# Optimization experiments

Measured on AMD Instinct MI355X. Metric: run time of the kernel, lower is better.

## Reference

```python
import jax, jax.numpy as jnp
import numpy as np

B, T, D = 2, 2048, 2048
H, KV, DH = 16, 8, 128
N, W, K = 1024, 256, 8


def rotate_half(x):
    x1, x2 = x[..., : DH // 2], x[..., DH // 2 :]
    return jnp.concatenate((-x2, x1), axis=-1)


def setup_inputs() -> dict:
    key = jax.random.key(0)
    ks = jax.random.split(key, 10)
    hidden_states = jax.random.normal(ks[0], (B, T, D), dtype=jnp.float32)
    cos = jax.random.uniform(ks[1], (B, T, DH), dtype=jnp.float32, minval=-1.0, maxval=1.0)
    sin = jax.random.uniform(ks[2], (B, T, DH), dtype=jnp.float32, minval=-1.0, maxval=1.0)
    mem = jax.random.normal(ks[3], (B, N, D), dtype=jnp.float32)
    Wq = jax.random.normal(ks[4], (D, D), dtype=jnp.float32) * 0.02
    Wk = jax.random.normal(ks[5], (KV * DH, D), dtype=jnp.float32) * 0.02
    Wv = jax.random.normal(ks[6], (KV * DH, D), dtype=jnp.float32) * 0.02
    Wo = jax.random.normal(ks[7], (D, D), dtype=jnp.float32) * 0.02
    Wg = jnp.zeros((1, D), dtype=jnp.float32)          # module inits gate weight to zeros
    bg = jnp.full((1,), 2.0, dtype=jnp.float32)        # and gate bias to 2.0
    return dict(hidden_states=hidden_states, cos=cos, sin=sin, mem=mem,
                Wq=Wq, Wk=Wk, Wv=Wv, Wo=Wo, Wg=Wg, bg=bg)


def reference(hidden_states, cos, sin, mem, Wq, Wk, Wv, Wo, Wg, bg):
    scale = DH ** -0.5
    n_rep = H // KV
    # projections -> [B, heads, T, d_h]
    q = (hidden_states @ Wq.T).reshape(B, T, H, DH).transpose(0, 2, 1, 3)
    k = (hidden_states @ Wk.T).reshape(B, T, KV, DH).transpose(0, 2, 1, 3)
    v = (hidden_states @ Wv.T).reshape(B, T, KV, DH).transpose(0, 2, 1, 3)
    # rotary (cos/sin are [B,T,d_h] -> broadcast over heads)
    c, s = cos[:, None], sin[:, None]
    q = q * c + rotate_half(q) * s
    k = k * c + rotate_half(k) * s
    # GQA repeat kv heads
    k_local = jnp.repeat(k, n_rep, axis=1)
    v_local = jnp.repeat(v, n_rep, axis=1)
    # --- local sliding-window causal attention (dense TxT mask, as in SDPA path) ---
    row = jnp.arange(T)[:, None]
    col = jnp.arange(T)[None, :]
    allowed = (col <= row) & (col >= row - W + 1)
    bias = jnp.where(allowed, 0.0, -jnp.inf).astype(q.dtype)
    scores = jnp.einsum('bhtd,bhsd->bhts', q, k_local) * scale + bias
    o_local = jnp.einsum('bhts,bhsd->bhtd', jax.nn.softmax(scores, axis=-1), v_local)
    o_local = o_local.transpose(0, 2, 1, 3).reshape(B, T, D) @ Wo.T
    # --- memory retrieval path (memory is detached in the original) ---
    mem_c = jax.lax.stop_gradient(mem)
    k_mem = (mem_c @ Wk.T).reshape(B, N, KV, DH).transpose(0, 2, 1, 3)
    v_mem = (mem_c @ Wv.T).reshape(B, N, KV, DH).transpose(0, 2, 1, 3)
    k_mem = jnp.repeat(k_mem, n_rep, axis=1)  # [B,H,N,d_h]
    v_mem = jnp.repeat(v_mem, n_rep, axis=1)
    q_chunk = q.mean(axis=2)                  # [B,H,d_h]
    sim_chunk = jnp.einsum('bhd,bhnd->bhn', q_chunk, k_mem) * scale
    _, idx = jax.lax.top_k(sim_chunk, K)      # [B,H,K]
    k_sh = jnp.take_along_axis(k_mem, idx[..., None], axis=2)  # [B,H,K,d_h]
    v_sh = jnp.take_along_axis(v_mem, idx[..., None], axis=2)
    sim_tok = jnp.einsum('bhtd,bhkd->bhtk', q, k_sh) * scale
    o_mem = jnp.einsum('bhtk,bhkd->bhtd', jax.nn.softmax(sim_tok, axis=-1), v_sh)
    o_mem = o_mem.transpose(0, 2, 1, 3).reshape(B, T, D)
    # --- learned gate fusion ---
    g = jax.nn.sigmoid(hidden_states @ Wg.T + bg)  # [B,T,1]
    return g * o_local + (1.0 - g) * o_mem
```

## Files before the change

kernel.cpp:

```cpp
#include <hip/hip_runtime.h>
#include <stdint.h>

#define B_   2
#define T_   2048
#define D_   2048
#define H_   16
#define KV_  8
#define DH_  128
#define NMEM 1024
#define WWIN 256
#define KSEL 8
#define BT   (B_*T_)
#define QKVSTR 4096

__constant__ const float kScale = 0.08838834764831845f;

typedef __attribute__((ext_vector_type(8))) short s16x8;
typedef __attribute__((ext_vector_type(4))) float f32x4;

__device__ inline unsigned short f2bf(float f) {
  union { float f; unsigned int u; } c; c.f = f;
  unsigned int u = c.u;
  unsigned int r = u + 0x7fffu + ((u >> 16) & 1u);
  return (unsigned short)(r >> 16);
}
__device__ inline float bf2f(unsigned short v) {
  union { unsigned int u; float f; } c; c.u = ((unsigned int)v) << 16;
  return c.f;
}
__device__ inline f32x4 fzero4() { f32x4 v; v[0]=0.f; v[1]=0.f; v[2]=0.f; v[3]=0.f; return v; }

__global__ __launch_bounds__(256) void conv_kernel(const float* __restrict__ src,
                                                   unsigned short* __restrict__ dst, int n) {
  int i = blockIdx.x * 256 + threadIdx.x;
  if (i * 4 >= n) return;
  float4 v = ((const float4*)src)[i];
  uint2 o;
  o.x = (unsigned)f2bf(v.x) | ((unsigned)f2bf(v.y) << 16);
  o.y = (unsigned)f2bf(v.z) | ((unsigned)f2bf(v.w) << 16);
  ((uint2*)dst)[i] = o;
}

#define AOFF(buf, half) ((buf)*32768 + (half)*16384)
#define BOFF(buf, half) (65536 + (buf)*32768 + (half)*16384)

#define PH_MFMA(P, BF) \
  { \
    _Pragma("unroll") \
    for (int mi = 0; mi < 2; ++mi) { \
      _Pragma("unroll") \
      for (int ni = 0; ni < 4; ++ni) { \
        acc[P][mi][ni] = __builtin_amdgcn_mfma_f32_16x16x32_bf16(af[mi][0], BF[ni][0], acc[P][mi][ni], 0, 0, 0); \
        acc[P][mi][ni] = __builtin_amdgcn_mfma_f32_16x16x32_bf16(af[mi][1], BF[ni][1], acc[P][mi][ni], 0, 0, 0); \
      } \
    } \
  }

template<int MODE>
__global__ __launch_bounds__(512, 2) void gemm256(const unsigned short* __restrict__ A,
                                                  const unsigned short* __restrict__ Bw,
                                                  int N, int K, int lda, int ldc,
                                                  unsigned short* __restrict__ Cb,
                                                  const float* __restrict__ g,
                                                  const unsigned short* __restrict__ omem,
                                                  float* __restrict__ dout) {
  __shared__ __align__(16) char lds[131072];
  const int tid = threadIdx.x;
  const int wv = tid >> 6, lane = tid & 63;
  const int l15 = lane & 15, lg = lane >> 4;
  const int wr = wv >> 1, wc = wv & 1;
  const int gx = gridDim.x;
  const int nwg = gx * gridDim.y;
  const int flat = blockIdx.y * gx + blockIdx.x;
  const int chunk = nwg >> 3;
  const int wg = (flat & 7) * chunk + (flat >> 3);
  const int bx = wg % gx, by = wg / gx;
  const int m0 = by * 256, n0 = bx * 256;
  const int NT = K >> 6;

  auto stage_half = [&](const unsigned short* base, int stride, int row0, int koff, int ldsoff) {
#pragma unroll
    for (int ld = 0; ld < 2; ++ld) {
      int s = ld * 512 + tid;
      int row = s >> 3, cs = s & 7;
      int cg = cs ^ (row & 7);
      const unsigned short* src = base + (size_t)(row0 + row) * stride + koff + cg * 8;
      __builtin_amdgcn_global_load_lds((const __attribute__((address_space(1))) void*)src,
          (__attribute__((address_space(3))) void*)(lds + ldsoff + ld * 8192 + wv * 1024), 16, 0, 0);
    }
  };
  auto rdA = [&](int buf, int half, int mi, int kk) -> s16x8 {
    int r = wr * 32 + mi * 16 + l15;
    int slot = (kk * 4 + lg) ^ (r & 7);
    return *(const s16x8*)(lds + AOFF(buf, half) + r * 128 + slot * 16);
  };
  auto rdB = [&](int buf, int half, int ni, int kk) -> s16x8 {
    int r = wc * 64 + ni * 16 + l15;
    int slot = (kk * 4 + lg) ^ (r & 7);
    return *(const s16x8*)(lds + BOFF(buf, half) + r * 128 + slot * 16);
  };

  f32x4 acc[4][2][4];
#pragma unroll
  for (int p = 0; p < 4; ++p)
#pragma unroll
    for (int mi = 0; mi < 2; ++mi)
#pragma unroll
      for (int ni = 0; ni < 4; ++ni) acc[p][mi][ni] = fzero4();

  stage_half(A,  lda, m0,       0,  AOFF(0, 0));
  stage_half(Bw, K,   n0,       0,  BOFF(0, 0));
  stage_half(A,  lda, m0 + 128, 0,  AOFF(0, 1));
  stage_half(Bw, K,   n0 + 128, 0,  BOFF(0, 1));
  stage_half(A,  lda, m0,       64, AOFF(1, 0));
  stage_half(Bw, K,   n0,       64, BOFF(1, 0));
  stage_half(A,  lda, m0 + 128, 64, AOFF(1, 1));
  asm volatile("s_waitcnt vmcnt(6)" ::: "memory");
  __builtin_amdgcn_s_barrier();

  int cur = 0;
  for (int t = 0; t < NT; ++t, cur ^= 1) {
    const int nxt = cur ^ 1;
    s16x8 af[2][2], b0f[4][2], b1f[4][2];
#pragma unroll
    for (int mi = 0; mi < 2; ++mi) {
      af[mi][0] = rdA(cur, 0, mi, 0);
      af[mi][1] = rdA(cur, 0, mi, 1);
    }
#pragma unroll
    for (int ni = 0; ni < 4; ++ni) {
      b0f[ni][0] = rdB(cur, 0, ni, 0);
      b0f[ni][1] = rdB(cur, 0, ni, 1);
    }
    if (t + 1 < NT) stage_half(Bw, K, n0 + 128, (t + 1) * 64, BOFF(nxt, 1));
    __builtin_amdgcn_s_barrier();
    asm volatile("s_waitcnt lgkmcnt(0)" ::: "memory");
    __builtin_amdgcn_s_setprio(1);
    PH_MFMA(0, b0f);
    __builtin_amdgcn_s_setprio(0);
    __builtin_amdgcn_s_barrier();
#pragma unroll
    for (int ni = 0; ni < 4; ++ni) {
      b1f[ni][0] = rdB(cur, 1, ni, 0);
      b1f[ni][1] = rdB(cur, 1, ni, 1);
    }
    if (t + 2 < NT) stage_half(A, lda, m0, (t + 2) * 64, AOFF(cur, 0));
    __builtin_amdgcn_s_barrier();
    asm volatile("s_waitcnt lgkmcnt(0)" ::: "memory");
    __builtin_amdgcn_s_setprio(1);
    PH_MFMA(1, b1f);
    __builtin_amdgcn_s_setprio(0);
    __builtin_amdgcn_s_barrier();
#pragma unroll
    for (int mi = 0; mi < 2; ++mi) {
      af[mi][0] = rdA(cur, 1, mi, 0);
      af[mi][1] = rdA(cur, 1, mi, 1);
    }
    if (t + 2 < NT) stage_half(Bw, K, n0, (t + 2) * 64, BOFF(cur, 0));
    __builtin_amdgcn_s_barrier();
    asm volatile("s_waitcnt lgkmcnt(0)" ::: "memory");
    __builtin_amdgcn_s_setprio(1);
    PH_MFMA(2, b0f);
    __builtin_amdgcn_s_setprio(0);
    __builtin_amdgcn_s_barrier();
    if (t + 2 < NT) stage_half(A, lda, m0 + 128, (t + 2) * 64, AOFF(cur, 1));
    __builtin_amdgcn_s_barrier();
    asm volatile("s_waitcnt lgkmcnt(0)" ::: "memory");
    __builtin_amdgcn_s_setprio(1);
    PH_MFMA(3, b1f);
    __builtin_amdgcn_s_setprio(0);
    if (t < NT - 2) asm volatile("s_waitcnt vmcnt(6)" ::: "memory");
    else            asm volatile("s_waitcnt vmcnt(0)" ::: "memory");
    __builtin_amdgcn_s_barrier();
  }

#pragma unroll
  for (int p = 0; p < 4; ++p)
#pragma unroll
    for (int mi = 0; mi < 2; ++mi)
#pragma unroll
      for (int ni = 0; ni < 4; ++ni)
#pragma unroll
        for (int j = 0; j < 4; ++j) {
          int row_g = m0 + (p >> 1) * 128 + wr * 32 + mi * 16 + lg * 4 + j;
          int col_g = n0 + (p & 1) * 128 + wc * 64 + ni * 16 + l15;
          float v = acc[p][mi][ni][j];
          size_t o = (size_t)row_g * ldc + col_g;
          if constexpr (MODE == 0) {
            Cb[o] = f2bf(v);
          } else {
            float gv = g[row_g];
            dout[o] = gv * v + (1.f - gv) * bf2f(omem[o]);
          }
        }
}

#define B2OFF(buf) (65536 + (buf)*16384)

__global__ __launch_bounds__(512, 2) void gemm256n(const unsigned short* __restrict__ A,
                                                   const unsigned short* __restrict__ Bw,
                                                   int N, int K, int lda, int ldc,
                                                   const float* __restrict__ g,
                                                   const unsigned short* __restrict__ omem,
                                                   float* __restrict__ dout) {
  __shared__ __align__(16) char lds[98304];
  const int tid = threadIdx.x;
  const int wv = tid >> 6, lane = tid & 63;
  const int l15 = lane & 15, lg = lane >> 4;
  const int wr = wv >> 1, wc = wv & 1;
  const int gx = gridDim.x;
  const int nwg = gx * gridDim.y;
  const int flat = blockIdx.y * gx + blockIdx.x;
  const int chunk = nwg >> 3;
  const int wg = (flat & 7) * chunk + (flat >> 3);
  const int bx = wg % gx, by = wg / gx;
  const int m0 = by * 256, n0 = bx * 128;
  const int NT = K >> 6;

  auto stage_half = [&](const unsigned short* base, int stride, int row0, int koff, int ldsoff) {
#pragma unroll
    for (int ld = 0; ld < 2; ++ld) {
      int s = ld * 512 + tid;
      int row = s >> 3, cs = s & 7;
      int cg = cs ^ (row & 7);
      const unsigned short* src = base + (size_t)(row0 + row) * stride + koff + cg * 8;
      __builtin_amdgcn_global_load_lds((const __attribute__((address_space(1))) void*)src,
          (__attribute__((address_space(3))) void*)(lds + ldsoff + ld * 8192 + wv * 1024), 16, 0, 0);
    }
  };
  auto rdA = [&](int buf, int half, int mi, int kk) -> s16x8 {
    int r = wr * 32 + mi * 16 + l15;
    int slot = (kk * 4 + lg) ^ (r & 7);
    return *(const s16x8*)(lds + AOFF(buf, half) + r * 128 + slot * 16);
  };
  auto rdB = [&](int buf, int ni, int kk) -> s16x8 {
    int r = wc * 64 + ni * 16 + l15;
    int slot = (kk * 4 + lg) ^ (r & 7);
    return *(const s16x8*)(lds + B2OFF(buf) + r * 128 + slot * 16);
  };

  f32x4 acc[2][2][4];
#pragma unroll
  for (int p = 0; p < 2; ++p)
#pragma unroll
    for (int mi = 0; mi < 2; ++mi)
#pragma unroll
      for (int ni = 0; ni < 4; ++ni) acc[p][mi][ni] = fzero4();

  stage_half(A,  lda, m0,       0,  AOFF(0, 0));
  stage_half(Bw, K,   n0,       0,  B2OFF(0));
  stage_half(A,  lda, m0 + 128, 0,  AOFF(0, 1));
  stage_half(A,  lda, m0,       64, AOFF(1, 0));
  stage_half(Bw, K,   n0,       64, B2OFF(1));
  asm volatile("s_waitcnt vmcnt(4)" ::: "memory");
  __builtin_amdgcn_s_barrier();

  int cur = 0;
  for (int t = 0; t < NT; ++t, cur ^= 1) {
    const int nxt = cur ^ 1;
    s16x8 af[2][2], b0f[4][2];
#pragma unroll
    for (int mi = 0; mi < 2; ++mi) {
      af[mi][0] = rdA(cur, 0, mi, 0);
      af[mi][1] = rdA(cur, 0, mi, 1);
    }
#pragma unroll
    for (int ni = 0; ni < 4; ++ni) {
      b0f[ni][0] = rdB(cur, ni, 0);
      b0f[ni][1] = rdB(cur, ni, 1);
    }
    if (t + 1 < NT) stage_half(A, lda, m0 + 128, (t + 1) * 64, AOFF(nxt, 1));
    __builtin_amdgcn_s_barrier();
    asm volatile("s_waitcnt lgkmcnt(0)" ::: "memory");
    __builtin_amdgcn_s_setprio(1);
    PH_MFMA(0, b0f);
    __builtin_amdgcn_s_setprio(0);
    __builtin_amdgcn_s_barrier();
#pragma unroll
    for (int mi = 0; mi < 2; ++mi) {
      af[mi][0] = rdA(cur, 1, mi, 0);
      af[mi][1] = rdA(cur, 1, mi, 1);
    }
    if (t + 2 < NT) {
      stage_half(A,  lda, m0, (t + 2) * 64, AOFF(cur, 0));
      stage_half(Bw, K,   n0, (t + 2) * 64, B2OFF(cur));
    }
    __builtin_amdgcn_s_barrier();
    asm volatile("s_waitcnt lgkmcnt(0)" ::: "memory");
    __builtin_amdgcn_s_setprio(1);
    PH_MFMA(1, b0f);
    __builtin_amdgcn_s_setprio(0);
    if (t < NT - 2) asm volatile("s_waitcnt vmcnt(4)" ::: "memory");
    else            asm volatile("s_waitcnt vmcnt(0)" ::: "memory");
    __builtin_amdgcn_s_barrier();
  }

#pragma unroll
  for (int p = 0; p < 2; ++p)
#pragma unroll
    for (int mi = 0; mi < 2; ++mi)
#pragma unroll
      for (int ni = 0; ni < 4; ++ni)
#pragma unroll
        for (int j = 0; j < 4; ++j) {
          int row_g = m0 + p * 128 + wr * 32 + mi * 16 + lg * 4 + j;
          int col_g = n0 + wc * 64 + ni * 16 + l15;
          float v = acc[p][mi][ni][j];
          size_t o = (size_t)row_g * ldc + col_g;
          float gv = g[row_g];
          dout[o] = gv * v + (1.f - gv) * bf2f(omem[o]);
        }
}

__global__ __launch_bounds__(256) void gsel_kernel(const unsigned short* __restrict__ mem_bf,
                                                   const unsigned short* __restrict__ wkv,
                                                   const int* __restrict__ idx,
                                                   float* __restrict__ kshp,
                                                   float* __restrict__ vshp) {
  __shared__ __align__(16) unsigned short selA[16][2056];
  __shared__ int selL[8];
  const int tid = threadIdx.x;
  const int h = blockIdx.x, b = blockIdx.y;
  const int kvh = h >> 1;
  if (tid < 8) selL[tid] = idx[(b * H_ + h) * KSEL + tid];
  __syncthreads();
#pragma unroll
  for (int it = 0; it < 8; ++it) {
    int i = it * 256 + tid;
    int r = i >> 8, c8 = i & 255;
    *(s16x8*)&selA[r][c8 * 8] =
        *(const s16x8*)(mem_bf + ((size_t)(b * NMEM + selL[r])) * D_ + c8 * 8);
  }
  {
    s16x8 z = {0, 0, 0, 0, 0, 0, 0, 0};
#pragma unroll
    for (int it = 0; it < 8; ++it) {
      int i = it * 256 + tid;
      int r = 8 + (i >> 8), c8 = i & 255;
      *(s16x8*)&selA[r][c8 * 8] = z;
    }
  }
  __syncthreads();
  const int w = tid >> 6, lane = tid & 63;
  const int l15 = lane & 15, lg = lane >> 4;
  f32x4 acc[4];
#pragma unroll
  for (int ni = 0; ni < 4; ++ni) acc[ni] = fzero4();
  const unsigned short* brow[4];
#pragma unroll
  for (int ni = 0; ni < 4; ++ni) {
    int col = w * 64 + ni * 16 + l15;
    brow[ni] = (col < 128)
        ? (wkv + (size_t)(kvh * DH_ + col) * D_)
        : (wkv + (size_t)(KV_ * DH_ + kvh * DH_ + (col - 128)) * D_);
  }
  for (int kt = 0; kt < D_ / 32; ++kt) {
    s16x8 af = *(const s16x8*)&selA[l15][kt * 32 + lg * 8];
#pragma unroll
    for (int ni = 0; ni < 4; ++ni) {
      s16x8 bf_ = *(const s16x8*)(brow[ni] + kt * 32 + lg * 8);
      acc[ni] = __builtin_amdgcn_mfma_f32_16x16x32_bf16(af, bf_, acc[ni], 0, 0, 0);
    }
  }
#pragma unroll
  for (int ni = 0; ni < 4; ++ni)
#pragma unroll
    for (int j = 0; j < 4; ++j) {
      int row = lg * 4 + j;
      int col = w * 64 + ni * 16 + l15;
      if (row < 8) {
        float* outp = (col < 128 ? kshp : vshp) +
                      ((size_t)(b * H_ + h) * KSEL + row) * DH_ + (col & 127);
        *outp = acc[ni][j];
      }
    }
}

__global__ __launch_bounds__(256) void rope_ip_kernel(unsigned short* __restrict__ buf,
                                                      const float* __restrict__ cosp,
                                                      const float* __restrict__ sinp,
                                                      int logp, int stride, int nthreads) {
  int i = blockIdx.x * 256 + threadIdx.x;
  if (i >= nthreads) return;
  int pp = i * 8;
  int row = pp >> logp;
  int p0 = pp & ((1 << logp) - 1);
  int blk = p0 >> 6, dd0 = p0 & 63;
  int b = row >> 11, t = row & 2047;
  const float* cb = cosp + ((size_t)b * T_ + t) * DH_;
  const float* sb = sinp + ((size_t)b * T_ + t) * DH_;
  unsigned short* p1 = buf + (size_t)row * stride + blk * 128 + dd0;
  s16x8 a = *(s16x8*)p1;
  s16x8 b8 = *(s16x8*)(p1 + 64);
  s16x8 o1, o2;
#pragma unroll
  for (int e = 0; e < 8; ++e) {
    float c1 = cb[dd0 + e], s1 = sb[dd0 + e];
    float c2 = cb[dd0 + 64 + e], s2 = sb[dd0 + 64 + e];
    float x1 = bf2f((unsigned short)a[e]), x2 = bf2f((unsigned short)b8[e]);
    o1[e] = (short)f2bf(x1 * c1 - x2 * s1);
    o2[e] = (short)f2bf(x2 * c2 + x1 * s2);
  }
  *(s16x8*)p1 = o1;
  *(s16x8*)(p1 + 64) = o2;
}

__global__ __launch_bounds__(256) void cs_kernel(const float* __restrict__ hs,
                                                 const float* __restrict__ cosp,
                                                 const float* __restrict__ sinp,
                                                 float* __restrict__ Cp, float* __restrict__ Sp) {
  __shared__ __align__(16) float hsL[32][128];
  __shared__ __align__(16) float csL[32][32];
  __shared__ __align__(16) float snL[32][32];
  const int tid = threadIdx.x;
  const int j0 = blockIdx.x * 128, d0 = blockIdx.y * 32;
  const int b = blockIdx.z >> 3, sp = blockIdx.z & 7;
  const int dq = (tid & 7) * 4;
  const int jq = (tid >> 3) * 4;
  float4 aC[4], aS[4];
#pragma unroll
  for (int a = 0; a < 4; ++a) {
    aC[a] = make_float4(0.f, 0.f, 0.f, 0.f);
    aS[a] = make_float4(0.f, 0.f, 0.f, 0.f);
  }
  const int csrow = tid >> 3, csc4 = tid & 7;
  for (int tile = 0; tile < 8; ++tile) {
    int t0 = sp * 256 + tile * 32;
    const float4* hs4 = (const float4*)(hs + ((size_t)b * T_ + t0) * D_ + j0);
#pragma unroll
    for (int r = 0; r < 4; ++r) {
      int i = tid + r * 256;
      int row = i >> 5, c4 = i & 31;
      *(float4*)&hsL[row][c4 * 4] = hs4[(size_t)row * (D_ / 4) + c4];
    }
    const float4* cp4 = (const float4*)(cosp + ((size_t)b * T_ + t0) * DH_ + d0);
    const float4* sp4 = (const float4*)(sinp + ((size_t)b * T_ + t0) * DH_ + d0);
    *(float4*)&csL[csrow][csc4 * 4] = cp4[(size_t)csrow * (DH_ / 4) + csc4];
    *(float4*)&snL[csrow][csc4 * 4] = sp4[(size_t)csrow * (DH_ / 4) + csc4];
    __syncthreads();
#pragma unroll 8
    for (int tt = 0; tt < 32; ++tt) {
      float4 cv = *(const float4*)&csL[tt][dq];
      float4 sv = *(const float4*)&snL[tt][dq];
      float4 hv = *(const float4*)&hsL[tt][jq];
      float ca[4] = {cv.x, cv.y, cv.z, cv.w};
      float sa[4] = {sv.x, sv.y, sv.z, sv.w};
#pragma unroll
      for (int a = 0; a < 4; ++a) {
        aC[a].x += ca[a] * hv.x; aC[a].y += ca[a] * hv.y;
        aC[a].z += ca[a] * hv.z; aC[a].w += ca[a] * hv.w;
        aS[a].x += sa[a] * hv.x; aS[a].y += sa[a] * hv.y;
        aS[a].z += sa[a] * hv.z; aS[a].w += sa[a] * hv.w;
      }
    }
    __syncthreads();
  }
#pragma unroll
  for (int a = 0; a < 4; ++a) {
    size_t o = ((size_t)(sp * B_ + b) * DH_ + d0 + dq + a) * D_ + j0 + jq;
    *(float4*)&Cp[o] = aC[a];
    *(float4*)&Sp[o] = aS[a];
  }
}

__global__ __launch_bounds__(256) void reduce_cs_kernel(const float4* __restrict__ Cp,
                                                        const float4* __restrict__ Sp,
                                                        float4* __restrict__ Cr,
                                                        float4* __restrict__ Sr) {
  int i = blockIdx.x * 256 + threadIdx.x;
  const int str = (B_ * DH_ * D_) / 4;
  float4 c = Cp[i], s = Sp[i];
#pragma unroll
  for (int p = 1; p < 8; ++p) {
    float4 cp = Cp[i + (size_t)p * str], sq = Sp[i + (size_t)p * str];
    c.x += cp.x; c.y += cp.y; c.z += cp.z; c.w += cp.w;
    s.x += sq.x; s.y += sq.y; s.z += sq.z; s.w += sq.w;
  }
  Cr[i] = c; Sr[i] = s;
}

__global__ __launch_bounds__(256) void qchunk_kernel(const float* __restrict__ Wq,
                                                     const float* __restrict__ Cr,
                                                     const float* __restrict__ Sr,
                                                     float* __restrict__ qc) {
  int gid = blockIdx.x * 256 + threadIdx.x;
  int wid = gid >> 6, lane = gid & 63;
  int b = wid >> 11, rem = wid & 2047;
  int h = rem >> 7, d = rem & 127;
  const float* w1 = Wq + (size_t)(h * DH_ + d) * D_;
  int dp = (d < 64) ? d + 64 : d - 64;
  float sgn = (d < 64) ? -1.f : 1.f;
  const float* w2 = Wq + (size_t)(h * DH_ + dp) * D_;
  const float* crow = Cr + ((size_t)b * DH_ + d) * D_;
  const float* srow = Sr + ((size_t)b * DH_ + d) * D_;
  float a1 = 0.f, a2 = 0.f;
  for (int j = lane; j < D_; j += 64) { a1 += w1[j] * crow[j]; a2 += w2[j] * srow[j]; }
#pragma unroll
  for (int off = 1; off < 64; off <<= 1) { a1 += __shfl_xor(a1, off); a2 += __shfl_xor(a2, off); }
  if (lane == 0) qc[wid] = (a1 + sgn * a2) * (1.f / (float)T_);
}

__global__ __launch_bounds__(256) void zk_kernel(const float* __restrict__ qc,
                                                 const float* __restrict__ Wk,
                                                 float* __restrict__ z) {
  int j = blockIdx.x * 256 + threadIdx.x;
  int h = blockIdx.y, b = blockIdx.z;
  int kvh = h >> 1;
  const float* qcl = qc + ((size_t)b * H_ + h) * DH_;
  const float* wb = Wk + (size_t)kvh * DH_ * D_ + j;
  float acc = 0.f;
#pragma unroll 8
  for (int d = 0; d < 128; ++d) acc += qcl[d] * wb[(size_t)d * D_];
  z[((size_t)b * H_ + h) * D_ + j] = acc;
}

__global__ __launch_bounds__(256) void sim_kernel(const float* __restrict__ z,
                                                  const float* __restrict__ mem,
                                                  float* __restrict__ sim) {
  __shared__ float4 mL[16 * 512];
  int tid = threadIdx.x;
  int n0 = blockIdx.x * 16, b = blockIdx.y;
  const float4* mem4 = (const float4*)(mem + (size_t)b * NMEM * D_);
#pragma unroll
  for (int c = 0; c < 32; ++c) {
    int i = tid + c * 256;
    int r = i >> 9, j4 = i & 511;
    mL[r * 512 + (j4 ^ (r & 7))] = mem4[(size_t)(n0 + r) * 512 + j4];
  }
  __syncthreads();
  int h = tid >> 4, n = tid & 15;
  const float4* zr = (const float4*)(z + ((size_t)b * H_ + h) * D_);
  float acc = 0.f;
  for (int j4 = 0; j4 < 512; ++j4) {
    float4 zz = zr[j4];
    float4 mm = mL[n * 512 + (j4 ^ (n & 7))];
    acc += zz.x * mm.x + zz.y * mm.y + zz.z * mm.z + zz.w * mm.w;
  }
  sim[((size_t)b * H_ + h) * NMEM + n0 + n] = acc * kScale;
}

__global__ __launch_bounds__(256) void topk_kernel(const float* __restrict__ sim,
                                                   int* __restrict__ idx) {
  __shared__ float sL[1024];
  __shared__ float rv[256];
  __shared__ int ri[256];
  int tid = threadIdx.x;
  int h = blockIdx.x, b = blockIdx.y;
  const float* sp = sim + ((size_t)b * H_ + h) * NMEM;
#pragma unroll
  for (int r = 0; r < 4; ++r) sL[tid + r * 256] = sp[tid + r * 256];
  __syncthreads();
  for (int kk = 0; kk < 8; ++kk) {
    float bv = -INFINITY; int bi = 0x7fffffff;
#pragma unroll
    for (int r = 0; r < 4; ++r) {
      int i = tid + r * 256;
      float v = sL[i];
      if (v > bv || (v == bv && i < bi)) { bv = v; bi = i; }
    }
    rv[tid] = bv; ri[tid] = bi;
    __syncthreads();
    for (int s = 128; s > 0; s >>= 1) {
      if (tid < s) {
        float v2 = rv[tid + s]; int i2 = ri[tid + s];
        if (v2 > rv[tid] || (v2 == rv[tid] && i2 < ri[tid])) { rv[tid] = v2; ri[tid] = i2; }
      }
      __syncthreads();
    }
    if (tid == 0) { idx[((size_t)b * H_ + h) * KSEL + kk] = ri[0]; sL[ri[0]] = -INFINITY; }
    __syncthreads();
  }
}

__global__ __launch_bounds__(256) void memattn_kernel(const unsigned short* __restrict__ qbf,
                                                      const float* __restrict__ ksh,
                                                      const float* __restrict__ vsh,
                                                      unsigned short* __restrict__ omem) {
  __shared__ float kl[8][128];
  __shared__ float vl[8][128];
  int tid = threadIdx.x;
  int b = blockIdx.z, h = blockIdx.y, t = blockIdx.x * 256 + tid;
  const float* ks = ksh + ((size_t)b * H_ + h) * KSEL * DH_;
  const float* vs = vsh + ((size_t)b * H_ + h) * KSEL * DH_;
#pragma unroll
  for (int r = 0; r < 4; ++r) {
    int i = tid + r * 256;
    ((float*)kl)[i] = ks[i];
    ((float*)vl)[i] = vs[i];
  }
  __syncthreads();
  float sc[8] = {0.f,0.f,0.f,0.f,0.f,0.f,0.f,0.f};
  const unsigned short* qr = qbf + (size_t)(b * T_ + t) * QKVSTR + h * DH_;
  for (int c = 0; c < 4; ++c) {
    const s16x8* qp = (const s16x8*)(qr + c * 32);
#pragma unroll
    for (int u = 0; u < 4; ++u) {
      s16x8 q8 = qp[u];
#pragma unroll
      for (int e = 0; e < 8; ++e) {
        float qv = bf2f((unsigned short)q8[e]);
        int d = c * 32 + u * 8 + e;
#pragma unroll
        for (int kk = 0; kk < 8; ++kk) sc[kk] += qv * kl[kk][d];
      }
    }
  }
  float sm[8], mx = -INFINITY;
#pragma unroll
  for (int kk = 0; kk < 8; ++kk) { sm[kk] = sc[kk] * kScale; mx = fmaxf(mx, sm[kk]); }
  float sum = 0.f;
#pragma unroll
  for (int kk = 0; kk < 8; ++kk) { sm[kk] = __expf(sm[kk] - mx); sum += sm[kk]; }
  float inv = 1.f / sum;
#pragma unroll
  for (int kk = 0; kk < 8; ++kk) sm[kk] *= inv;
  unsigned short* orow = omem + (size_t)(b * T_ + t) * D_ + h * DH_;
  for (int d = 0; d < 128; d += 4) {
    float o0 = 0.f, o1 = 0.f, o2 = 0.f, o3 = 0.f;
#pragma unroll
    for (int kk = 0; kk < 8; ++kk) {
      float w = sm[kk];
      o0 += w * vl[kk][d + 0];
      o1 += w * vl[kk][d + 1];
      o2 += w * vl[kk][d + 2];
      o3 += w * vl[kk][d + 3];
    }
    uint2 pk;
    pk.x = (unsigned)f2bf(o0) | ((unsigned)f2bf(o1) << 16);
    pk.y = (unsigned)f2bf(o2) | ((unsigned)f2bf(o3) << 16);
    *(uint2*)(orow + d) = pk;
  }
}

__global__ __launch_bounds__(256) void gate_kernel(const float* __restrict__ hs,
                                                   const float* __restrict__ Wg,
                                                   const float* __restrict__ bg,
                                                   float* __restrict__ g) {
  int gid = blockIdx.x * 256 + threadIdx.x;
  int row = gid >> 6, lane = gid & 63;
  const float4* hr = (const float4*)(hs + (size_t)row * D_);
  const float4* wg4 = (const float4*)Wg;
  float acc = 0.f;
#pragma unroll
  for (int it = 0; it < 8; ++it) {
    float4 hv = hr[lane + it * 64], wv = wg4[lane + it * 64];
    acc += hv.x * wv.x + hv.y * wv.y + hv.z * wv.z + hv.w * wv.w;
  }
#pragma unroll
  for (int off = 1; off < 64; off <<= 1) acc += __shfl_xor(acc, off);
  if (lane == 0) g[row] = 1.f / (1.f + __expf(-(acc + bg[0])));
}

__global__ __launch_bounds__(256) void localattn_kernel(const unsigned short* __restrict__ qbf,
                                                        const unsigned short* __restrict__ kbf,
                                                        const unsigned short* __restrict__ vbf,
                                                        unsigned short* __restrict__ olocal) {
  __shared__ __align__(16) unsigned short kL[2][32][128];
  __shared__ __align__(16) unsigned short vL[2][128][32];
  __shared__ __align__(16) unsigned short pl[4][16][40];
  const int tid = threadIdx.x;
  const int w = tid >> 6, lane = tid & 63;
  const int tb = blockIdx.x * 64;
  const int h = blockIdx.y, b = blockIdx.z;
  const int kvh = h >> 1;
  const int t0 = tb + w * 16;
  const int l15 = lane & 15, lg = lane >> 4;

  s16x8 qf[4];
  {
    const unsigned short* qb = qbf + ((size_t)(b * T_ + t0 + l15) * QKVSTR) + h * DH_ + lg * 8;
#pragma unroll
    for (int kb = 0; kb < 4; ++kb) qf[kb] = *(const s16x8*)(qb + kb * 32);
  }
  f32x4 of[8];
#pragma unroll
  for (int nb = 0; nb < 8; ++nb) of[nb] = fzero4();
  float m_r[4] = {-INFINITY, -INFINITY, -INFINITY, -INFINITY};
  float l_r[4] = {0.f, 0.f, 0.f, 0.f};

  int sstart = tb - (WWIN - 1);
  if (sstart < 0) sstart = 0;
  sstart &= ~31;
  const int slast = tb + 63;

  const int vk = tid & 15, vcg = tid >> 4;
  auto STAGE = [&](int buf, int s0) {
#pragma unroll
    for (int ld = 0; ld < 2; ++ld) {
      int s = ld * 256 + tid;
      int r = s >> 4, cs = s & 15;
      int cg = cs ^ (r & 7);
      const unsigned short* src = kbf + (size_t)(b * T_ + s0 + r) * QKVSTR + kvh * DH_ + cg * 8;
      __builtin_amdgcn_global_load_lds((const __attribute__((address_space(1))) void*)src,
          (__attribute__((address_space(3))) void*)((char*)&kL[buf][0][0] + ld * 4096 + w * 1024), 16, 0, 0);
    }
    {
      int r0 = 2 * vk;
      const unsigned short* vs = vbf + (size_t)(b * T_ + s0 + r0) * QKVSTR + kvh * DH_ + vcg * 8;
      s16x8 va = *(const s16x8*)vs;
      s16x8 vb2 = *(const s16x8*)(vs + QKVSTR);
      int q = vk >> 2;
      int colbase = 2 * (vk & 3);
#pragma unroll
      for (int e = 0; e < 8; ++e) {
        int c = vcg * 8 + e;
        int blk = q ^ ((c >> 2) & 3);
        unsigned int val = (unsigned int)(unsigned short)va[e] |
                           ((unsigned int)(unsigned short)vb2[e] << 16);
        *(unsigned int*)&vL[buf][c][blk * 8 + colbase] = val;
      }
    }
  };

  STAGE(0, sstart);
  int buf = 0;
  const int vp = (l15 >> 2) & 3;
  for (int s0 = sstart; s0 <= slast; s0 += 32, buf ^= 1) {
    __syncthreads();
    if (s0 + 32 <= slast) STAGE(buf ^ 1, s0 + 32);

    f32x4 sc[2];
    sc[0] = fzero4(); sc[1] = fzero4();
#pragma unroll
    for (int cb = 0; cb < 2; ++cb) {
#pragma unroll
      for (int kb = 0; kb < 4; ++kb) {
        int r = cb * 16 + l15;
        int c = kb * 4 + lg;
        s16x8 kf = *(const s16x8*)((char*)&kL[buf][0][0] + r * 256 + ((c ^ (r & 7)) * 16));
        sc[cb] = __builtin_amdgcn_mfma_f32_16x16x32_bf16(qf[kb], kf, sc[cb], 0, 0, 0);
      }
    }
    float pv[2][4];
#pragma unroll
    for (int j = 0; j < 4; ++j) {
      int t = t0 + lg * 4 + j;
      int s_a = s0 + l15, s_b = s_a + 16;
      float va = sc[0][j] * kScale;
      float vb = sc[1][j] * kScale;
      va = (s_a <= t && s_a + (WWIN - 1) >= t) ? va : -INFINITY;
      vb = (s_b <= t && s_b + (WWIN - 1) >= t) ? vb : -INFINITY;
      float mx = fmaxf(va, vb);
#pragma unroll
      for (int off = 1; off < 16; off <<= 1) mx = fmaxf(mx, __shfl_xor(mx, off));
      float mn = fmaxf(m_r[j], mx);
      float alpha, pa, pb;
      if (mn == -INFINITY) { alpha = 1.f; pa = 0.f; pb = 0.f; }
      else {
        alpha = __expf(m_r[j] - mn);
        pa = __expf(va - mn);
        pb = __expf(vb - mn);
      }
      m_r[j] = mn;
      float rs = pa + pb;
#pragma unroll
      for (int off = 1; off < 16; off <<= 1) rs += __shfl_xor(rs, off);
      l_r[j] = l_r[j] * alpha + rs;
#pragma unroll
      for (int nb = 0; nb < 8; ++nb) of[nb][j] *= alpha;
      pv[0][j] = pa; pv[1][j] = pb;
    }
#pragma unroll
    for (int cb = 0; cb < 2; ++cb)
#pragma unroll
      for (int j = 0; j < 4; ++j)
        pl[w][lg * 4 + j][cb * 16 + l15] = f2bf(pv[cb][j]);
    asm volatile("s_waitcnt lgkmcnt(0)" ::: "memory");
    __builtin_amdgcn_sched_barrier(0);
    s16x8 pa8 = *(const s16x8*)&pl[w][l15][lg * 8];
#pragma unroll
    for (int nb = 0; nb < 8; ++nb) {
      int c = nb * 16 + l15;
      s16x8 vf = *(const s16x8*)&vL[buf][c][(lg ^ vp) * 8];
      of[nb] = __builtin_amdgcn_mfma_f32_16x16x32_bf16(pa8, vf, of[nb], 0, 0, 0);
    }
  }

  float inv[4];
#pragma unroll
  for (int j = 0; j < 4; ++j) inv[j] = 1.f / l_r[j];
#pragma unroll
  for (int nb = 0; nb < 8; ++nb)
#pragma unroll
    for (int j = 0; j < 4; ++j) {
      int t = t0 + lg * 4 + j;
      olocal[(size_t)(b * T_ + t) * QKVSTR + h * DH_ + nb * 16 + l15] = f2bf(of[nb][j] * inv[j]);
    }
}

extern "C" void kernel_launch(void* const* d_in, const int* in_sizes, int n_in,
                              void* d_out, int out_size, void* d_ws, size_t ws_size,
                              hipStream_t stream) {
  const float* hs   = (const float*)d_in[0];
  const float* cosp = (const float*)d_in[1];
  const float* sinp = (const float*)d_in[2];
  const float* mem  = (const float*)d_in[3];
  const float* Wq   = (const float*)d_in[4];
  const float* Wk   = (const float*)d_in[5];
  const float* Wv   = (const float*)d_in[6];
  const float* Wo   = (const float*)d_in[7];
  const float* Wg   = (const float*)d_in[8];
  const float* bg   = (const float*)d_in[9];
  float* out = (float*)d_out;

  char* p = (char*)d_ws;
  auto alloc = [&](size_t bytes) { char* r = p; p += (bytes + 255) & ~(size_t)255; return r; };
  float* qc     = (float*)alloc((size_t)B_ * H_ * DH_ * 4);
  float* gbuf   = (float*)alloc((size_t)BT * 4);
  float* zbuf   = (float*)alloc((size_t)B_ * H_ * D_ * 4);
  float* simbuf = (float*)alloc((size_t)B_ * H_ * NMEM * 4);
  int*   idxbuf = (int*)alloc((size_t)B_ * H_ * KSEL * 4);
  float* ksh    = (float*)alloc((size_t)B_ * H_ * KSEL * DH_ * 4);
  float* vsh    = (float*)alloc((size_t)B_ * H_ * KSEL * DH_ * 4);
  unsigned short* hs_bf   = (unsigned short*)alloc((size_t)BT * D_ * 2);
  unsigned short* qkv_raw = (unsigned short*)alloc((size_t)BT * QKVSTR * 2);
  unsigned short* wbig    = (unsigned short*)alloc((size_t)2 * D_ * D_ * 2);
  unsigned short* mem_bf  = (unsigned short*)alloc((size_t)B_ * NMEM * D_ * 2);
  float* crsr             = (float*)alloc((size_t)2 * B_ * DH_ * D_ * 4);

  float* Cp = (float*)d_out;
  float* Sp = Cp + (size_t)8 * B_ * DH_ * D_;
  float* Cr = crsr;
  float* Sr = Cr + (size_t)B_ * DH_ * D_;
  unsigned short* omem_bf = hs_bf;

  conv_kernel<<<(BT * D_ / 4 + 255) / 256, 256, 0, stream>>>(hs, hs_bf, BT * D_);
  conv_kernel<<<(D_ * D_ / 4 + 255) / 256, 256, 0, stream>>>(Wq, wbig, D_ * D_);
  conv_kernel<<<(KV_ * DH_ * D_ / 4 + 255) / 256, 256, 0, stream>>>(Wk, wbig + (size_t)D_ * D_, KV_ * DH_ * D_);
  conv_kernel<<<(KV_ * DH_ * D_ / 4 + 255) / 256, 256, 0, stream>>>(Wv, wbig + (size_t)D_ * D_ + (size_t)KV_ * DH_ * D_, KV_ * DH_ * D_);
  gemm256<0><<<dim3(QKVSTR / 256, BT / 256), 512, 0, stream>>>(hs_bf, wbig, QKVSTR, D_, D_, QKVSTR, qkv_raw, nullptr, nullptr, nullptr);
  conv_kernel<<<(B_ * NMEM * D_ / 4 + 255) / 256, 256, 0, stream>>>(mem, mem_bf, B_ * NMEM * D_);

  rope_ip_kernel<<<(BT * D_ / 16 + 255) / 256, 256, 0, stream>>>(qkv_raw, cosp, sinp, 10, QKVSTR, BT * D_ / 16);
  rope_ip_kernel<<<(BT * KV_ * DH_ / 16 + 255) / 256, 256, 0, stream>>>(qkv_raw + D_, cosp, sinp, 9, QKVSTR, BT * KV_ * DH_ / 16);

  cs_kernel<<<dim3(D_ / 128, DH_ / 32, B_ * 8), 256, 0, stream>>>(hs, cosp, sinp, Cp, Sp);
  reduce_cs_kernel<<<(B_ * DH_ * D_ / 4) / 256, 256, 0, stream>>>((const float4*)Cp, (const float4*)Sp, (float4*)Cr, (float4*)Sr);
  qchunk_kernel<<<(B_ * H_ * DH_) / 4, 256, 0, stream>>>(Wq, Cr, Sr, qc);
  zk_kernel<<<dim3(D_ / 256, H_, B_), 256, 0, stream>>>(qc, Wk, zbuf);
  sim_kernel<<<dim3(NMEM / 16, B_), 256, 0, stream>>>(zbuf, mem, simbuf);
  topk_kernel<<<dim3(H_, B_), 256, 0, stream>>>(simbuf, idxbuf);

  gsel_kernel<<<dim3(H_, B_), 256, 0, stream>>>(mem_bf, wbig + (size_t)D_ * D_, idxbuf, ksh, vsh);
  memattn_kernel<<<dim3(T_ / 256, H_, B_), 256, 0, stream>>>(qkv_raw, ksh, vsh, omem_bf);

  gate_kernel<<<BT / 4, 256, 0, stream>>>(hs, Wg, bg, gbuf);

  localattn_kernel<<<dim3(T_ / 64, H_, B_), 256, 0, stream>>>(qkv_raw, qkv_raw + D_, qkv_raw + D_ + KV_ * DH_, qkv_raw);

  conv_kernel<<<(D_ * D_ / 4 + 255) / 256, 256, 0, stream>>>(Wo, wbig, D_ * D_);
  gemm256n<<<dim3(D_ / 128, BT / 256), 512, 0, stream>>>(qkv_raw, wbig, D_, D_, QKVSTR, D_, gbuf, omem_bf, out);
}
```

Baseline: 402.2 us.

## Retile cos/sin projection kernel and skip out-of-window tiles per wave in local attention

The cs_kernel now has each block cover 64 d-columns and 512 timesteps, and each thread computes a 4x8 output tile instead of 4x4. This halves the number of partial sums and the work left for the reduction kernel. Separately, in local attention each wave skips the QK/softmax/PV MFMAs for key tiles that fall outside its own 16-row window, while the block still stages the full block-wide range. Together these target wasted matrix work and reduction traffic, at the cost of more registers in cs_kernel and fewer blocks launched.

```diff
diff --git a/kernel.cpp b/kernel.cpp
--- a/kernel.cpp
+++ b/kernel.cpp
@@ -410,22 +410,23 @@
                                                  const float* __restrict__ sinp,
                                                  float* __restrict__ Cp, float* __restrict__ Sp) {
   __shared__ __align__(16) float hsL[32][128];
-  __shared__ __align__(16) float csL[32][32];
-  __shared__ __align__(16) float snL[32][32];
+  __shared__ __align__(16) float csL[32][64];
+  __shared__ __align__(16) float snL[32][64];
   const int tid = threadIdx.x;
-  const int j0 = blockIdx.x * 128, d0 = blockIdx.y * 32;
-  const int b = blockIdx.z >> 3, sp = blockIdx.z & 7;
-  const int dq = (tid & 7) * 4;
-  const int jq = (tid >> 3) * 4;
-  float4 aC[4], aS[4];
-#pragma unroll
-  for (int a = 0; a < 4; ++a) {
-    aC[a] = make_float4(0.f, 0.f, 0.f, 0.f);
-    aS[a] = make_float4(0.f, 0.f, 0.f, 0.f);
-  }
-  const int csrow = tid >> 3, csc4 = tid & 7;
-  for (int tile = 0; tile < 8; ++tile) {
-    int t0 = sp * 256 + tile * 32;
+  const int j0 = blockIdx.x * 128, d0 = blockIdx.y * 64;
+  const int b = blockIdx.z >> 2, sp = blockIdx.z & 3;
+  const int dq = (tid & 15) * 4;
+  const int jq = (tid >> 4) * 8;
+  float4 aC[4][2], aS[4][2];
+#pragma unroll
+  for (int a = 0; a < 4; ++a)
+#pragma unroll
+    for (int hh = 0; hh < 2; ++hh) {
+      aC[a][hh] = make_float4(0.f, 0.f, 0.f, 0.f);
+      aS[a][hh] = make_float4(0.f, 0.f, 0.f, 0.f);
+    }
+  for (int tile = 0; tile < 16; ++tile) {
+    int t0 = sp * 512 + tile * 32;
     const float4* hs4 = (const float4*)(hs + ((size_t)b * T_ + t0) * D_ + j0);
 #pragma unroll
     for (int r = 0; r < 4; ++r) {
@@ -435,22 +436,32 @@
     }
     const float4* cp4 = (const float4*)(cosp + ((size_t)b * T_ + t0) * DH_ + d0);
     const float4* sp4 = (const float4*)(sinp + ((size_t)b * T_ + t0) * DH_ + d0);
-    *(float4*)&csL[csrow][csc4 * 4] = cp4[(size_t)csrow * (DH_ / 4) + csc4];
-    *(float4*)&snL[csrow][csc4 * 4] = sp4[(size_t)csrow * (DH_ / 4) + csc4];
+#pragma unroll
+    for (int r = 0; r < 2; ++r) {
+      int i = tid + r * 256;
+      int row = i >> 4, c4 = i & 15;
+      *(float4*)&csL[row][c4 * 4] = cp4[(size_t)row * (DH_ / 4) + c4];
+      *(float4*)&snL[row][c4 * 4] = sp4[(size_t)row * (DH_ / 4) + c4];
+    }
     __syncthreads();
-#pragma unroll 8
+#pragma unroll 4
     for (int tt = 0; tt < 32; ++tt) {
       float4 cv = *(const float4*)&csL[tt][dq];
       float4 sv = *(const float4*)&snL[tt][dq];
-      float4 hv = *(const float4*)&hsL[tt][jq];
+      float4 h0 = *(const float4*)&hsL[tt][jq];
+      float4 h1 = *(const float4*)&hsL[tt][jq + 4];
       float ca[4] = {cv.x, cv.y, cv.z, cv.w};
       float sa[4] = {sv.x, sv.y, sv.z, sv.w};
 #pragma unroll
       for (int a = 0; a < 4; ++a) {
-        aC[a].x += ca[a] * hv.x; aC[a].y += ca[a] * hv.y;
-        aC[a].z += ca[a] * hv.z; aC[a].w += ca[a] * hv.w;
-        aS[a].x += sa[a] * hv.x; aS[a].y += sa[a] * hv.y;
-        aS[a].z += sa[a] * hv.z; aS[a].w += sa[a] * hv.w;
+        aC[a][0].x += ca[a] * h0.x; aC[a][0].y += ca[a] * h0.y;
+        aC[a][0].z += ca[a] * h0.z; aC[a][0].w += ca[a] * h0.w;
+        aC[a][1].x += ca[a] * h1.x; aC[a][1].y += ca[a] * h1.y;
+        aC[a][1].z += ca[a] * h1.z; aC[a][1].w += ca[a] * h1.w;
+        aS[a][0].x += sa[a] * h0.x; aS[a][0].y += sa[a] * h0.y;
+        aS[a][0].z += sa[a] * h0.z; aS[a][0].w += sa[a] * h0.w;
+        aS[a][1].x += sa[a] * h1.x; aS[a][1].y += sa[a] * h1.y;
+        aS[a][1].z += sa[a] * h1.z; aS[a][1].w += sa[a] * h1.w;
       }
     }
     __syncthreads();
@@ -458,8 +469,10 @@
 #pragma unroll
   for (int a = 0; a < 4; ++a) {
     size_t o = ((size_t)(sp * B_ + b) * DH_ + d0 + dq + a) * D_ + j0 + jq;
-    *(float4*)&Cp[o] = aC[a];
-    *(float4*)&Sp[o] = aS[a];
+    *(float4*)&Cp[o] = aC[a][0];
+    *(float4*)&Cp[o + 4] = aC[a][1];
+    *(float4*)&Sp[o] = aS[a][0];
+    *(float4*)&Sp[o + 4] = aS[a][1];
   }
 }
 
@@ -471,7 +484,7 @@
   const int str = (B_ * DH_ * D_) / 4;
   float4 c = Cp[i], s = Sp[i];
 #pragma unroll
-  for (int p = 1; p < 8; ++p) {
+  for (int p = 1; p < 4; ++p) {
     float4 cp = Cp[i + (size_t)p * str], sq = Sp[i + (size_t)p * str];
     c.x += cp.x; c.y += cp.y; c.z += cp.z; c.w += cp.w;
     s.x += sq.x; s.y += sq.y; s.z += sq.z; s.w += sq.w;
@@ -682,6 +695,10 @@
   if (sstart < 0) sstart = 0;
   sstart &= ~31;
   const int slast = tb + 63;
+  int wlow = t0 - (WWIN - 1);
+  if (wlow < 0) wlow = 0;
+  wlow &= ~31;
+  const int whigh = t0 + 15;
 
   const int vk = tid & 15, vcg = tid >> 4;
   auto STAGE = [&](int buf, int s0) {
@@ -719,60 +736,62 @@
     __syncthreads();
     if (s0 + 32 <= slast) STAGE(buf ^ 1, s0 + 32);
 
-    f32x4 sc[2];
-    sc[0] = fzero4(); sc[1] = fzero4();
-#pragma unroll
-    for (int cb = 0; cb < 2; ++cb) {
-#pragma unroll
-      for (int kb = 0; kb < 4; ++kb) {
-        int r = cb * 16 + l15;
-        int c = kb * 4 + lg;
-        s16x8 kf = *(const s16x8*)((char*)&kL[buf][0][0] + r * 256 + ((c ^ (r & 7)) * 16));
-        sc[cb] = __builtin_amdgcn_mfma_f32_16x16x32_bf16(qf[kb], kf, sc[cb], 0, 0, 0);
+    if (s0 >= wlow && s0 <= whigh) {
+      f32x4 sc[2];
+      sc[0] = fzero4(); sc[1] = fzero4();
+#pragma unroll
+      for (int cb = 0; cb < 2; ++cb) {
+#pragma unroll
+        for (int kb = 0; kb < 4; ++kb) {
+          int r = cb * 16 + l15;
+          int c = kb * 4 + lg;
+          s16x8 kf = *(const s16x8*)((char*)&kL[buf][0][0] + r * 256 + ((c ^ (r & 7)) * 16));
+          sc[cb] = __builtin_amdgcn_mfma_f32_16x16x32_bf16(qf[kb], kf, sc[cb], 0, 0, 0);
+        }
       }
-    }
-    float pv[2][4];
-#pragma unroll
-    for (int j = 0; j < 4; ++j) {
-      int t = t0 + lg * 4 + j;
-      int s_a = s0 + l15, s_b = s_a + 16;
-      float va = sc[0][j] * kScale;
-      float vb = sc[1][j] * kScale;
-      va = (s_a <= t && s_a + (WWIN - 1) >= t) ? va : -INFINITY;
-      vb = (s_b <= t && s_b + (WWIN - 1) >= t) ? vb : -INFINITY;
-      float mx = fmaxf(va, vb);
-#pragma unroll
-      for (int off = 1; off < 16; off <<= 1) mx = fmaxf(mx, __shfl_xor(mx, off));
-      float mn = fmaxf(m_r[j], mx);
-      float alpha, pa, pb;
-      if (mn == -INFINITY) { alpha = 1.f; pa = 0.f; pb = 0.f; }
-      else {
-        alpha = __expf(m_r[j] - mn);
-        pa = __expf(va - mn);
-        pb = __expf(vb - mn);
+      float pv[2][4];
+#pragma unroll
+      for (int j = 0; j < 4; ++j) {
+        int t = t0 + lg * 4 + j;
+        int s_a = s0 + l15, s_b = s_a + 16;
+        float va = sc[0][j] * kScale;
+        float vb = sc[1][j] * kScale;
+        va = (s_a <= t && s_a + (WWIN - 1) >= t) ? va : -INFINITY;
+        vb = (s_b <= t && s_b + (WWIN - 1) >= t) ? vb : -INFINITY;
+        float mx = fmaxf(va, vb);
+#pragma unroll
+        for (int off = 1; off < 16; off <<= 1) mx = fmaxf(mx, __shfl_xor(mx, off));
+        float mn = fmaxf(m_r[j], mx);
+        float alpha, pa, pb;
+        if (mn == -INFINITY) { alpha = 1.f; pa = 0.f; pb = 0.f; }
+        else {
+          alpha = __expf(m_r[j] - mn);
+          pa = __expf(va - mn);
+          pb = __expf(vb - mn);
+        }
+        m_r[j] = mn;
+        float rs = pa + pb;
+#pragma unroll
+        for (int off = 1; off < 16; off <<= 1) rs += __shfl_xor(rs, off);
+        l_r[j] = l_r[j] * alpha + rs;
+#pragma unroll
+        for (int nb = 0; nb < 8; ++nb) of[nb][j] *= alpha;
+        pv[0][j] = pa; pv[1][j] = pb;
       }
-      m_r[j] = mn;
-      float rs = pa + pb;
-#pragma unroll
-      for (int off = 1; off < 16; off <<= 1) rs += __shfl_xor(rs, off);
-      l_r[j] = l_r[j] * alpha + rs;
-#pragma unroll
-      for (int nb = 0; nb < 8; ++nb) of[nb][j] *= alpha;
-      pv[0][j] = pa; pv[1][j] = pb;
-    }
-#pragma unroll
-    for (int cb = 0; cb < 2; ++cb)
-#pragma unroll
-      for (int j = 0; j < 4; ++j)
-        pl[w][lg * 4 + j][cb * 16 + l15] = f2bf(pv[cb][j]);
-    asm volatile("s_waitcnt lgkmcnt(0)" ::: "memory");
-    __builtin_amdgcn_sched_barrier(0);
-    s16x8 pa8 = *(const s16x8*)&pl[w][l15][lg * 8];
-#pragma unroll
-    for (int nb = 0; nb < 8; ++nb) {
-      int c = nb * 16 + l15;
-      s16x8 vf = *(const s16x8*)&vL[buf][c][(lg ^ vp) * 8];
-      of[nb] = __builtin_amdgcn_mfma_f32_16x16x32_bf16(pa8, vf, of[nb], 0, 0, 0);
+#pragma unroll
+      for (int cb = 0; cb < 2; ++cb)
+#pragma unroll
+        for (int j = 0; j < 4; ++j)
+          pl[w][lg * 4 + j][cb * 16 + l15] = f2bf(pv[cb][j]);
+      asm volatile("s_waitcnt lgkmcnt(0)" ::: "memory");
+      __builtin_amdgcn_sched_barrier(0);
+      s16x8 pa8 = *(const s16x8*)&pl[w][l15][lg * 8];
+#pragma unroll
+      for (int nb = 0; nb < 8; ++nb) {
+        int c = nb * 16 + l15;
+        s16x8 vf = *(const s16x8*)&vL[buf][c][(lg ^ vp) * 8];
+        of[nb] = __builtin_amdgcn_mfma_f32_16x16x32_bf16(pa8, vf, of[nb], 0, 0, 0);
+      }
     }
   }
 
@@ -819,7 +838,7 @@
   float* crsr             = (float*)alloc((size_t)2 * B_ * DH_ * D_ * 4);
 
   float* Cp = (float*)d_out;
-  float* Sp = Cp + (size_t)8 * B_ * DH_ * D_;
+  float* Sp = Cp + (size_t)4 * B_ * DH_ * D_;
   float* Cr = crsr;
   float* Sr = Cr + (size_t)B_ * DH_ * D_;
   unsigned short* omem_bf = hs_bf;
@@ -834,7 +853,7 @@
   rope_ip_kernel<<<(BT * D_ / 16 + 255) / 256, 256, 0, stream>>>(qkv_raw, cosp, sinp, 10, QKVSTR, BT * D_ / 16);
   rope_ip_kernel<<<(BT * KV_ * DH_ / 16 + 255) / 256, 256, 0, stream>>>(qkv_raw + D_, cosp, sinp, 9, QKVSTR, BT * KV_ * DH_ / 16);
 
-  cs_kernel<<<dim3(D_ / 128, DH_ / 32, B_ * 8), 256, 0, stream>>>(hs, cosp, sinp, Cp, Sp);
+  cs_kernel<<<dim3(D_ / 128, DH_ / 64, B_ * 4), 256, 0, stream>>>(hs, cosp, sinp, Cp, Sp);
   reduce_cs_kernel<<<(B_ * DH_ * D_ / 4) / 256, 256, 0, stream>>>((const float4*)Cp, (const float4*)Sp, (float4*)Cr, (float4*)Sr);
   qchunk_kernel<<<(B_ * H_ * DH_) / 4, 256, 0, stream>>>(Wq, Cr, Sr, qc);
   zk_kernel<<<dim3(D_ / 256, H_, B_), 256, 0, stream>>>(qc, Wk, zbuf);
```

Result: slower. 433.9 us (+7.9%).
